# Optimization experiments

Hardware: AMD Instinct MI355X
Metric: run time of the kernel (lower is better)

Reference implementation:

```python
import math
import jax, jax.numpy as jnp
import numpy as np

BSZ, SEQ, DIM = 2, 2048, 4096
N_HEADS, N_KV = 32, 8
HEAD_DIM = DIM // N_HEADS  # 128
N_REP = N_HEADS // N_KV    # 4
EPS = 1e-5
ROPE_THETA = 500000.0


def setup_inputs() -> dict:
    key = jax.random.key(0)
    ks = jax.random.split(key, 6)
    scale = 0.02
    x = jax.random.normal(ks[0], (BSZ, SEQ, DIM), dtype=jnp.float32)
    wq = jax.random.normal(ks[1], (N_HEADS * HEAD_DIM, DIM), dtype=jnp.float32) * scale
    wk = jax.random.normal(ks[2], (N_KV * HEAD_DIM, DIM), dtype=jnp.float32) * scale
    wv = jax.random.normal(ks[3], (N_KV * HEAD_DIM, DIM), dtype=jnp.float32) * scale
    wo = jax.random.normal(ks[4], (N_HEADS * HEAD_DIM, DIM), dtype=jnp.float32).T * scale  # [DIM, n_heads*hd] -> stored as [out,in]
    wo = jax.random.normal(ks[4], (DIM, N_HEADS * HEAD_DIM), dtype=jnp.float32) * scale
    # RoPE tables (real/imag parts of freqs_cis)
    inv_freq = 1.0 / (ROPE_THETA ** (jnp.arange(0, HEAD_DIM, 2, dtype=jnp.float32) / HEAD_DIM))
    angles = jnp.arange(SEQ, dtype=jnp.float32)[:, None] * inv_freq[None, :]  # [SEQ, HEAD_DIM//2]
    cos, sin = jnp.cos(angles), jnp.sin(angles)
    # causal additive mask
    neg_inf = jnp.finfo(jnp.float32).min
    mask = jnp.where(jnp.tril(jnp.ones((SEQ, SEQ), dtype=bool)), 0.0, neg_inf).astype(jnp.float32)
    return {"x": x, "wq": wq, "wk": wk, "wv": wv, "wo": wo,
            "cos": cos, "sin": sin, "mask": mask, "start_pos": 0}


def _apply_rope(t, cos, sin):
    # t: [b, s, h, hd]; pairs (even, odd) as in view_as_complex
    tf = t.astype(jnp.float32).reshape(*t.shape[:-1], HEAD_DIM // 2, 2)
    e, o = tf[..., 0], tf[..., 1]
    c = cos[None, :, None, :]
    s = sin[None, :, None, :]
    out = jnp.stack([e * c - o * s, e * s + o * c], axis=-1)
    return out.reshape(t.shape).astype(t.dtype)


def _rmsnorm(t):
    tf = t.astype(jnp.float32)
    return (tf * jax.lax.rsqrt(jnp.mean(tf * tf, axis=-1, keepdims=True) + EPS)).astype(t.dtype)


def reference(x, wq, wk, wv, wo, cos, sin, mask, start_pos):
    b, s, _ = x.shape
    xq = (x @ wq.T).reshape(b, s, N_HEADS, HEAD_DIM)
    xk = (x @ wk.T).reshape(b, s, N_KV, HEAD_DIM)
    xv = (x @ wv.T).reshape(b, s, N_KV, HEAD_DIM)
    xq = _apply_rope(xq, cos, sin)
    xk = _apply_rope(xk, cos, sin)
    xq = _rmsnorm(xq)
    xk = _rmsnorm(xk)
    # KV cache write/read with start_pos=0 over seqlen tokens is identity here.
    # GQA without repeat_interleave: q head h attends kv head h // N_REP
    q = xq.transpose(0, 2, 1, 3).reshape(b, N_KV, N_REP, s, HEAD_DIM)
    k = xk.transpose(0, 2, 1, 3)  # [b, n_kv, s, hd]
    v = xv.transpose(0, 2, 1, 3)
    scale = 1.0 / math.sqrt(HEAD_DIM)
    scores = jnp.einsum('bgrqd,bgkd->bgrqk', q, k) * scale + mask[None, None, None]
    probs = jax.nn.softmax(scores, axis=-1)
    out = jnp.einsum('bgrqk,bgkd->bgrqd', probs, v)
    out = out.reshape(b, N_HEADS, s, HEAD_DIM).transpose(0, 2, 1, 3).reshape(b, s, N_HEADS * HEAD_DIM)
    return out @ wo.T
```

## Files before the change

kernel.cpp:

```cpp
#include <hip/hip_runtime.h>
#include <hip/hip_bf16.h>
#include <stdint.h>

#define SEQ 2048
#define DIMSZ 4096
#define QKVN 6144

typedef __attribute__((ext_vector_type(8))) __bf16 bf16x8;
typedef __attribute__((ext_vector_type(4))) float f32x4;

static __device__ __forceinline__ void gld_lds16(const void* g, void* l) {
  __builtin_amdgcn_global_load_lds(
      (__attribute__((address_space(1))) void*)(g),
      (__attribute__((address_space(3))) void*)(l), 16, 0, 0);
}

__global__ __launch_bounds__(256) void k_cvt(const float* __restrict__ in,
                                             __bf16* __restrict__ out, long n) {
  long i = (long)blockIdx.x * 256 + threadIdx.x;
  long stride = (long)gridDim.x * 256;
  for (long e = i * 8; e < n; e += stride * 8) {
    float4 v0 = *(const float4*)(in + e);
    float4 v1 = *(const float4*)(in + e + 4);
    bf16x8 o;
    o[0] = (__bf16)v0.x; o[1] = (__bf16)v0.y; o[2] = (__bf16)v0.z; o[3] = (__bf16)v0.w;
    o[4] = (__bf16)v1.x; o[5] = (__bf16)v1.y; o[6] = (__bf16)v1.z; o[7] = (__bf16)v1.w;
    *(bf16x8*)(out + e) = o;
  }
}

template <typename OutT>
__global__ __launch_bounds__(256) void k_gemm128(const __bf16* __restrict__ A,
                                                 const __bf16* __restrict__ B,
                                                 OutT* __restrict__ C,
                                                 int M, int N, int K) {
  __shared__ __bf16 As[128 * 32];
  __shared__ __bf16 Bs[128 * 32];
  const int t = threadIdx.x;
  const int l = t & 63;
  const int w = t >> 6;
  const int wr = w >> 1, wc = w & 1;
  const int lr = l & 15, lg = l >> 4;
  const int rsw = (lr >> 1) & 3;
  const int bm = blockIdx.y, bn = blockIdx.x;

  const int scol = (((t & 3) ^ ((t >> 3) & 3)) << 3);
  const __bf16* pa0 = A + (size_t)(bm * 128 + (t >> 2)) * K + scol;
  const __bf16* pa1 = pa0 + (size_t)64 * K;
  const __bf16* pb0 = B + (size_t)(bn * 128 + (t >> 2)) * K + scol;
  const __bf16* pb1 = pb0 + (size_t)64 * K;
  const int ldst = t * 8;

  const int aoff = (wr * 64 + lr) * 32 + ((lg ^ rsw) * 8);
  const int boff = (wc * 64 + lr) * 32 + ((lg ^ rsw) * 8);

  f32x4 acc[4][4] = {};
  const int nt = K >> 5;

  for (int kt = 0; kt < nt; ++kt) {
    __syncthreads();
    gld_lds16(pa0, &As[ldst]);
    gld_lds16(pa1, &As[2048 + ldst]);
    gld_lds16(pb0, &Bs[ldst]);
    gld_lds16(pb1, &Bs[2048 + ldst]);
    pa0 += 32; pa1 += 32; pb0 += 32; pb1 += 32;
    __syncthreads();

    bf16x8 a[4], b[4];
#pragma unroll
    for (int mi = 0; mi < 4; ++mi)
      a[mi] = *(const bf16x8*)&As[aoff + mi * 512];
#pragma unroll
    for (int ni = 0; ni < 4; ++ni)
      b[ni] = *(const bf16x8*)&Bs[boff + ni * 512];
#pragma unroll
    for (int mi = 0; mi < 4; ++mi)
#pragma unroll
      for (int ni = 0; ni < 4; ++ni)
        acc[mi][ni] = __builtin_amdgcn_mfma_f32_16x16x32_bf16(a[mi], b[ni], acc[mi][ni], 0, 0, 0);
  }

  const int row0 = bm * 128 + wr * 64;
  const int col0 = bn * 128 + wc * 64;
#pragma unroll
  for (int mi = 0; mi < 4; ++mi)
#pragma unroll
    for (int ni = 0; ni < 4; ++ni)
#pragma unroll
      for (int r = 0; r < 4; ++r)
        C[(size_t)(row0 + mi * 16 + lg * 4 + r) * N + (col0 + ni * 16 + lr)] =
            (OutT)acc[mi][ni][r];
}

__global__ __launch_bounds__(256) void k_rope_norm(__bf16* __restrict__ qkv,
                                                   const float* __restrict__ cosT,
                                                   const float* __restrict__ sinT) {
  const int task = blockIdx.x * 4 + (threadIdx.x >> 6);
  const int l = threadIdx.x & 63;
  const int m = task / 40;
  const int h = task - m * 40;
  const int s = m & (SEQ - 1);
  const bool isQ = h < 32;
  const int col = isQ ? h * 128 : 4096 + (h - 32) * 128;
  __bf16* p = qkv + (size_t)m * QKVN + col + l * 2;
  float e = (float)p[0], o = (float)p[1];
  float c = cosT[s * 64 + l], sn = sinT[s * 64 + l];
  float e2 = e * c - o * sn;
  float o2 = e * sn + o * c;
  float ss = e2 * e2 + o2 * o2;
#pragma unroll
  for (int off = 32; off > 0; off >>= 1) ss += __shfl_xor(ss, off);
  float r = rsqrtf(ss * (1.0f / 128.0f) + 1e-5f);
  if (isQ) r *= 0.08838834764831845f;
  p[0] = (__bf16)(e2 * r);
  p[1] = (__bf16)(o2 * r);
}

__global__ __launch_bounds__(256) void k_transpose_v(const __bf16* __restrict__ qkv,
                                                     __bf16* __restrict__ vt) {
  __shared__ __bf16 tile[64][136];
  const int t = threadIdx.x;
  const int st = blockIdx.x, bg = blockIdx.y;
  const int b = bg >> 3, g = bg & 7;
  const int s0 = st * 64;
#pragma unroll
  for (int p = 0; p < 4; ++p) {
    int row = p * 16 + (t >> 4);
    int co = (t & 15) * 8;
    *(bf16x8*)&tile[row][co] =
        *(const bf16x8*)&qkv[(size_t)(b * SEQ + s0 + row) * QKVN + 5120 + g * 128 + co];
  }
  __syncthreads();
#pragma unroll
  for (int p = 0; p < 4; ++p) {
    int d = p * 32 + (t >> 3);
    int so = (t & 7) * 8;
    bf16x8 v;
#pragma unroll
    for (int j = 0; j < 8; ++j) v[j] = tile[so + j][d];
    *(bf16x8*)&vt[((size_t)bg * 128 + d) * SEQ + s0 + so] = v;
  }
}

__global__ __launch_bounds__(256) void k_flash(const __bf16* __restrict__ qkv,
                                               const __bf16* __restrict__ vt,
                                               __bf16* __restrict__ attno) {
  __shared__ __bf16 Ks[64 * 128];
  __shared__ __bf16 Vs[128 * 64];
  __shared__ __bf16 Ps[4][16 * 64];
  const int t = threadIdx.x, w = t >> 6, l = t & 63;
  const int lr = l & 15, lg = l >> 4;
  const int bh = blockIdx.y;
  const int b = bh >> 5, h = bh & 31, g = h >> 2;
  const int qt0 = blockIdx.x, qt1 = 31 - (int)blockIdx.x;

  const __bf16* Kb = qkv + 4096 + (size_t)(b * SEQ) * QKVN + g * 128;
  const __bf16* Vtb = vt + ((size_t)(b * 8 + g)) * 128 * SEQ;
  const int wbase = (t & ~63) * 8;
  const int sw = lr & 7;

  for (int pass = 0; pass < 2; ++pass) {
    const int qt = (pass == 0) ? qt0 : qt1;

    const __bf16* Qb = qkv + (size_t)(b * SEQ + qt * 64 + w * 16 + lr) * QKVN + h * 128;
    bf16x8 qf[4];
#pragma unroll
    for (int kk = 0; kk < 4; ++kk) qf[kk] = *(const bf16x8*)&Qb[kk * 32 + lg * 8];

    f32x4 oacc[8] = {};
    float mrow[4], lsum[4];
#pragma unroll
    for (int r = 0; r < 4; ++r) { mrow[r] = -1e30f; lsum[r] = 0.f; }

    for (int kt = 0; kt <= qt; ++kt) {
      const int kv0 = kt * 64;
#pragma unroll
      for (int i = 0; i < 4; ++i) {
        int e = i * 256 + t;
        gld_lds16(Kb + (size_t)(kv0 + (e >> 4)) * QKVN + ((e & 15) ^ ((e >> 4) & 7)) * 8,
                  &Ks[i * 2048 + wbase]);
      }
#pragma unroll
      for (int i = 0; i < 4; ++i) {
        int e = i * 256 + t;
        gld_lds16(Vtb + (size_t)(e >> 3) * SEQ + kv0 + (((e & 7) ^ ((e >> 3) & 7))) * 8,
                  &Vs[i * 2048 + wbase]);
      }
      __syncthreads();

      f32x4 sc[4] = {};
#pragma unroll
      for (int kk = 0; kk < 4; ++kk)
#pragma unroll
        for (int n = 0; n < 4; ++n) {
          bf16x8 kf = *(const bf16x8*)&Ks[(n * 16 + lr) * 128 + ((kk * 4 + lg) ^ sw) * 8];
          sc[n] = __builtin_amdgcn_mfma_f32_16x16x32_bf16(qf[kk], kf, sc[n], 0, 0, 0);
        }

      if (kt == qt) {
#pragma unroll
        for (int n = 0; n < 4; ++n)
#pragma unroll
          for (int r = 0; r < 4; ++r)
            if (n * 16 + lr > w * 16 + lg * 4 + r) sc[n][r] = -1e30f;
      }

#pragma unroll
      for (int r = 0; r < 4; ++r) {
        float pm = fmaxf(fmaxf(sc[0][r], sc[1][r]), fmaxf(sc[2][r], sc[3][r]));
#pragma unroll
        for (int off = 8; off > 0; off >>= 1) pm = fmaxf(pm, __shfl_xor(pm, off));
        float mn = fmaxf(mrow[r], pm);
        float corr = __expf(mrow[r] - mn);
        mrow[r] = mn;
        float ps = 0.f;
#pragma unroll
        for (int n = 0; n < 4; ++n) { sc[n][r] = __expf(sc[n][r] - mn); ps += sc[n][r]; }
#pragma unroll
        for (int off = 8; off > 0; off >>= 1) ps += __shfl_xor(ps, off);
        lsum[r] = lsum[r] * corr + ps;
#pragma unroll
        for (int dn = 0; dn < 8; ++dn) oacc[dn][r] *= corr;
      }

#pragma unroll
      for (int n = 0; n < 4; ++n)
#pragma unroll
        for (int r = 0; r < 4; ++r) {
          int row = lg * 4 + r;
          Ps[w][row * 64 + (((n * 2 + (lr >> 3)) ^ (row & 7)) * 8) + (lr & 7)] = (__bf16)sc[n][r];
        }

#pragma unroll
      for (int ks = 0; ks < 2; ++ks) {
        bf16x8 pf = *(const bf16x8*)&Ps[w][lr * 64 + ((ks * 4 + lg) ^ sw) * 8];
#pragma unroll
        for (int dn = 0; dn < 8; ++dn) {
          bf16x8 vf = *(const bf16x8*)&Vs[(dn * 16 + lr) * 64 + ((ks * 4 + lg) ^ sw) * 8];
          oacc[dn] = __builtin_amdgcn_mfma_f32_16x16x32_bf16(pf, vf, oacc[dn], 0, 0, 0);
        }
      }
      __syncthreads();
    }

    __bf16* Ob = attno + (size_t)(b * SEQ + qt * 64 + w * 16) * DIMSZ + h * 128;
#pragma unroll
    for (int dn = 0; dn < 8; ++dn)
#pragma unroll
      for (int r = 0; r < 4; ++r)
        Ob[(size_t)(lg * 4 + r) * DIMSZ + dn * 16 + lr] = (__bf16)(oacc[dn][r] / lsum[r]);
  }
}

extern "C" void kernel_launch(void* const* d_in, const int* in_sizes, int n_in,
                              void* d_out, int out_size, void* d_ws, size_t ws_size,
                              hipStream_t stream) {
  const float* x    = (const float*)d_in[0];
  const float* wq   = (const float*)d_in[1];
  const float* wk   = (const float*)d_in[2];
  const float* wv   = (const float*)d_in[3];
  const float* wo   = (const float*)d_in[4];
  const float* cosT = (const float*)d_in[5];
  const float* sinT = (const float*)d_in[6];

  char* ws = (char*)d_ws;
  __bf16* xb    = (__bf16*)(ws);
  __bf16* wqkvb = (__bf16*)(ws + 33554432);
  __bf16* qkvb  = (__bf16*)(ws + 83886080);
  __bf16* wob   = (__bf16*)(ws + 134217728);
  __bf16* vt    = (__bf16*)(ws + 167772160);
  __bf16* attno = (__bf16*)(ws + 176160768);
  float* out = (float*)d_out;

  k_cvt<<<8192, 256, 0, stream>>>(x, xb, 16777216L);
  k_cvt<<<8192, 256, 0, stream>>>(wq, wqkvb, 16777216L);
  k_cvt<<<2048, 256, 0, stream>>>(wk, wqkvb + 16777216, 4194304L);
  k_cvt<<<2048, 256, 0, stream>>>(wv, wqkvb + 20971520, 4194304L);
  k_cvt<<<8192, 256, 0, stream>>>(wo, wob, 16777216L);

  k_gemm128<__bf16><<<dim3(48, 32), 256, 0, stream>>>(xb, wqkvb, qkvb, 4096, QKVN, 4096);
  k_rope_norm<<<40960, 256, 0, stream>>>(qkvb, cosT, sinT);
  k_transpose_v<<<dim3(32, 16), 256, 0, stream>>>(qkvb, vt);
  k_flash<<<dim3(16, 64), 256, 0, stream>>>(qkvb, vt, attno);
  k_gemm128<float><<<dim3(32, 32), 256, 0, stream>>>(attno, wob, out, 4096, DIMSZ, 4096);
}
```

Measured before the change: 720.7 us.

## Triple-buffer GEMM LDS tiles with async prefetch two stages ahead

Replaces the single-buffered load/sync/compute loop in the bf16 GEMM with a three-stage LDS ring. Global-to-LDS loads are issued two k-tiles ahead and waited on with a partial vmcnt. The aim is to overlap memory latency with MFMA work instead of stalling on every tile. LDS use triples to 48KB per block, which could limit occupancy. The hand-written waitcnt and barrier ordering must stay correct.

Result: faster. 675.1 us (-6.3%).

```diff
diff --git a/kernel.cpp b/kernel.cpp
--- a/kernel.cpp
+++ b/kernel.cpp
@@ -30,12 +30,12 @@
 }
 
 template <typename OutT>
-__global__ __launch_bounds__(256) void k_gemm128(const __bf16* __restrict__ A,
-                                                 const __bf16* __restrict__ B,
-                                                 OutT* __restrict__ C,
-                                                 int M, int N, int K) {
-  __shared__ __bf16 As[128 * 32];
-  __shared__ __bf16 Bs[128 * 32];
+__global__ __launch_bounds__(256, 3) void k_gemm128(const __bf16* __restrict__ A,
+                                                    const __bf16* __restrict__ B,
+                                                    OutT* __restrict__ C,
+                                                    int M, int N, int K) {
+  __shared__ __bf16 As[3][128 * 32];
+  __shared__ __bf16 Bs[3][128 * 32];
   const int t = threadIdx.x;
   const int l = t & 63;
   const int w = t >> 6;
@@ -57,27 +57,40 @@
   f32x4 acc[4][4] = {};
   const int nt = K >> 5;
 
+  gld_lds16(pa0, &As[0][ldst]);       gld_lds16(pa1, &As[0][2048 + ldst]);
+  gld_lds16(pb0, &Bs[0][ldst]);       gld_lds16(pb1, &Bs[0][2048 + ldst]);
+  gld_lds16(pa0 + 32, &As[1][ldst]);  gld_lds16(pa1 + 32, &As[1][2048 + ldst]);
+  gld_lds16(pb0 + 32, &Bs[1][ldst]);  gld_lds16(pb1 + 32, &Bs[1][2048 + ldst]);
+
+  int rb = 0, sb = 2;
   for (int kt = 0; kt < nt; ++kt) {
-    __syncthreads();
-    gld_lds16(pa0, &As[ldst]);
-    gld_lds16(pa1, &As[2048 + ldst]);
-    gld_lds16(pb0, &Bs[ldst]);
-    gld_lds16(pb1, &Bs[2048 + ldst]);
-    pa0 += 32; pa1 += 32; pb0 += 32; pb1 += 32;
-    __syncthreads();
+    const int kc = ((kt + 2 < nt) ? kt + 2 : nt - 1) << 5;
+    gld_lds16(pa0 + kc, &As[sb][ldst]);
+    gld_lds16(pa1 + kc, &As[sb][2048 + ldst]);
+    gld_lds16(pb0 + kc, &Bs[sb][ldst]);
+    gld_lds16(pb1 + kc, &Bs[sb][2048 + ldst]);
+
+    asm volatile("s_waitcnt vmcnt(8)" ::: "memory");
+    __builtin_amdgcn_s_barrier();
+    asm volatile("" ::: "memory");
 
     bf16x8 a[4], b[4];
 #pragma unroll
     for (int mi = 0; mi < 4; ++mi)
-      a[mi] = *(const bf16x8*)&As[aoff + mi * 512];
+      a[mi] = *(const bf16x8*)&As[rb][aoff + mi * 512];
 #pragma unroll
     for (int ni = 0; ni < 4; ++ni)
-      b[ni] = *(const bf16x8*)&Bs[boff + ni * 512];
+      b[ni] = *(const bf16x8*)&Bs[rb][boff + ni * 512];
 #pragma unroll
     for (int mi = 0; mi < 4; ++mi)
 #pragma unroll
       for (int ni = 0; ni < 4; ++ni)
         acc[mi][ni] = __builtin_amdgcn_mfma_f32_16x16x32_bf16(a[mi], b[ni], acc[mi][ni], 0, 0, 0);
+
+    asm volatile("" ::: "memory");
+    __builtin_amdgcn_s_barrier();
+    rb = (rb == 2) ? 0 : rb + 1;
+    sb = (sb == 2) ? 0 : sb + 1;
   }
 
   const int row0 = bm * 128 + wr * 64;
```
